# Optimization experiments

Hardware: AMD Instinct MI355X
Metric: run time of the kernel (lower is better)

## Reference

```python
import jax, jax.numpy as jnp
import numpy as np

N_NODES = 50000
N_FEAT = 256
HIDDEN = 256
N_EDGES = 800000


def gcn_conv(x, edge_index, W, b):
    """PyG GCNConv: out = D^-1/2 (A+I) D^-1/2 (x @ W) + b."""
    n = x.shape[0]
    loop = jnp.arange(n, dtype=edge_index.dtype)
    src = jnp.concatenate([edge_index[0], loop])  # [E+N]
    dst = jnp.concatenate([edge_index[1], loop])  # [E+N]
    deg = jax.ops.segment_sum(jnp.ones_like(dst, dtype=x.dtype), dst, num_segments=n)
    dinv = jnp.where(deg > 0, jax.lax.rsqrt(deg), 0.0)
    norm = dinv[src] * dinv[dst]                  # [E+N]
    h = x @ W                                     # [N, out]
    msg = h[src] * norm[:, None]                  # gather + scale
    out = jax.ops.segment_sum(msg, dst, num_segments=n)  # scatter-add
    return out + b


def setup_inputs() -> dict:
    key = jax.random.key(0)
    ks = jax.random.split(key, 8)
    x = jax.random.normal(ks[0], (N_NODES, N_FEAT), dtype=jnp.float32)
    train_pos_edge_index = jax.random.randint(ks[1], (2, N_EDGES), 0, N_NODES, dtype=jnp.int64)
    pos_edge_index = jax.random.randint(ks[2], (2, N_EDGES), 0, N_NODES, dtype=jnp.int64)
    neg_edge_index = jax.random.randint(ks[3], (2, N_EDGES), 0, N_NODES, dtype=jnp.int64)
    # Glorot-style init for GCN weights
    W1 = jax.random.normal(ks[4], (N_FEAT, HIDDEN), dtype=jnp.float32) * (1.0 / np.sqrt(N_FEAT))
    b1 = jnp.zeros((HIDDEN,), dtype=jnp.float32)
    W2 = jax.random.normal(ks[5], (HIDDEN, HIDDEN // 2), dtype=jnp.float32) * (1.0 / np.sqrt(HIDDEN))
    b2 = jnp.zeros((HIDDEN // 2,), dtype=jnp.float32)
    return {"x": x, "train_pos_edge_index": train_pos_edge_index,
            "pos_edge_index": pos_edge_index, "neg_edge_index": neg_edge_index,
            "W1": W1, "b1": b1, "W2": W2, "b2": b2}


def reference(x, train_pos_edge_index, pos_edge_index, neg_edge_index, W1, b1, W2, b2):
    # encode
    h = jax.nn.relu(gcn_conv(x, train_pos_edge_index, W1, b1))
    z = gcn_conv(h, train_pos_edge_index, W2, b2)  # [N, HIDDEN//2]
    # decode: dot product over concatenated pos+neg edges
    edge_index = jnp.concatenate([pos_edge_index, neg_edge_index], axis=-1)  # [2, 2E]
    logits = jnp.sum(z[edge_index[0]] * z[edge_index[1]], axis=-1)           # [2E]
    return logits
```

## Files before the change

### kernel.cpp

```cpp
#include <hip/hip_runtime.h>
#include <hip/hip_fp16.h>


#define NFEAT 256
#define HID   256
#define OUTF  128

typedef _Float16 f16x8 __attribute__((ext_vector_type(8)));
typedef _Float16 f16x2 __attribute__((ext_vector_type(2)));
typedef float    f32x4 __attribute__((ext_vector_type(4)));

__device__ __forceinline__ void wt_body(const float* __restrict__ W,
                                        __half* __restrict__ Wt,
                                        int K, int M, int bxx, int byy) {
    __shared__ float tile[32][33];
    int k0 = bxx * 32, m0 = byy * 32;
    int tx = threadIdx.x & 31, ty = threadIdx.x >> 5;
#pragma unroll
    for (int r = 0; r < 4; ++r)
        tile[ty + r * 8][tx] = W[(size_t)(k0 + ty + r * 8) * M + m0 + tx];
    __syncthreads();
#pragma unroll
    for (int r = 0; r < 4; ++r)
        Wt[(size_t)(m0 + ty + r * 8) * K + k0 + tx] = __float2half(tile[tx][ty + r * 8]);
}

__global__ __launch_bounds__(256) void k_prep(
        const float* __restrict__ W1, __half* __restrict__ W1t,
        const float* __restrict__ W2, __half* __restrict__ W2t,
        float* __restrict__ deg, int n) {
    int bid = blockIdx.x;
    if (bid < 64) { wt_body(W1, W1t, NFEAT, HID, bid & 7, bid >> 3); return; }
    bid -= 64;
    if (bid < 32) { wt_body(W2, W2t, HID, OUTF, bid & 7, bid >> 3); return; }
    bid -= 32;
    int i = bid * 256 + threadIdx.x;
    if (i < n) deg[i] = 1.0f;
}

__global__ void k_count_deg(const int* __restrict__ ei, float* __restrict__ deg, int E) {
    int e = blockIdx.x * blockDim.x + threadIdx.x;
    if (e < E) atomicAdd(&deg[ei[E + e]], 1.0f);
}

__global__ __launch_bounds__(1024) void k_scan1(
        const float* __restrict__ deg, int* __restrict__ excl,
        int* __restrict__ bsum, int n) {
    __shared__ int swsum[16];
    const int t = threadIdx.x, wave = t >> 6, lane = t & 63;
    const int i = blockIdx.x * 1024 + t;
    int v = (i < n) ? (int)deg[i] - 1 : 0;
    int sc = v;
#pragma unroll
    for (int off = 1; off < 64; off <<= 1) {
        int y = __shfl_up(sc, off);
        if (lane >= off) sc += y;
    }
    if (lane == 63) swsum[wave] = sc;
    __syncthreads();
    if (t < 16) {
        int w = swsum[t];
        int scw = w;
#pragma unroll
        for (int off = 1; off < 16; off <<= 1) {
            int y = __shfl_up(scw, off);
            if (t >= off) scw += y;
        }
        swsum[t] = scw - w;
        if (t == 15) bsum[blockIdx.x] = scw;
    }
    __syncthreads();
    if (i < n) excl[i] = swsum[wave] + (sc - v);
}

__global__ __launch_bounds__(256) void k_scan3(
        float* __restrict__ deg_dinv, const int* __restrict__ excl,
        const int* __restrict__ bsum, int* __restrict__ rowptr,
        int* __restrict__ cursor, int n, int nb) {
    __shared__ int pbs[65];
    const int t = threadIdx.x;
    if (t < 64) {
        int v = (t < nb) ? bsum[t] : 0;
        int sc = v;
#pragma unroll
        for (int off = 1; off < 64; off <<= 1) {
            int y = __shfl_up(sc, off);
            if (t >= off) sc += y;
        }
        pbs[t] = sc - v;
        if (t == 63) pbs[64] = sc;
    }
    __syncthreads();
    int i = blockIdx.x * 256 + t;
    if (i < n) {
        int rp = excl[i] + pbs[i >> 10];
        rowptr[i] = rp;
        cursor[i] = rp;
        deg_dinv[i] = rsqrtf(deg_dinv[i]);
    } else if (i == n) {
        rowptr[n] = pbs[64];
    }
}

__global__ void k_fill(const int* __restrict__ ei, int* __restrict__ cursor,
                       int* __restrict__ eidx, int E) {
    int e = blockIdx.x * blockDim.x + threadIdx.x;
    if (e < E) {
        int s = ei[e];
        int d = ei[E + e];
        int p = atomicAdd(&cursor[d], 1);
        eidx[p] = s;
    }
}

template <int MT, bool AF32, int SWL>
__global__ __launch_bounds__(256) void k_gemm_mfma(
        const void* __restrict__ Aptr, const __half* __restrict__ Wt,
        const float* __restrict__ dinv, __half* __restrict__ outp,
        int n, int K, int M) {
    constexpr int BM = 2 * MT * 16;
    __shared__ __half As[BM][40];
    __shared__ __half Bs[128][40];
    __shared__ __half Cs[4][16][72];

    const int t    = threadIdx.x;
    const int wave = t >> 6;
    const int lane = t & 63;
    const int row0 = blockIdx.x * BM;
    const int col0 = blockIdx.y * 128;
    const int wm = wave >> 1, wn = wave & 1;
    const int lr = lane & 15;
    const int kq = lane >> 4;

    f32x4 acc[MT][4];
#pragma unroll
    for (int i = 0; i < MT; ++i)
#pragma unroll
        for (int j = 0; j < 4; ++j) acc[i][j] = (f32x4){0.f, 0.f, 0.f, 0.f};

    for (int k0 = 0; k0 < K; k0 += 32) {
        if (AF32) {
            const float* A = (const float*)Aptr;
#pragma unroll
            for (int it = 0; it < BM * 8 / 256; ++it) {
                int q = t + it * 256;
                int r = q >> 3, c4 = q & 7;
                int gr = min(row0 + r, n - 1);
                float4 v = *(const float4*)&A[(size_t)gr * K + k0 + c4 * 4];
                __half2* dst = (__half2*)&As[r][c4 * 4];
                dst[0] = __floats2half2_rn(v.x, v.y);
                dst[1] = __floats2half2_rn(v.z, v.w);
            }
        } else {
            const __half* A = (const __half*)Aptr;
#pragma unroll
            for (int it = 0; it < BM * 4 / 256; ++it) {
                int q = t + it * 256;
                int r = q >> 2, c8 = q & 3;
                int gr = min(row0 + r, n - 1);
                *(float4*)&As[r][c8 * 8] = *(const float4*)&A[(size_t)gr * K + k0 + c8 * 8];
            }
        }
#pragma unroll
        for (int it = 0; it < 2; ++it) {
            int q = t + it * 256;
            int r = q >> 2, c8 = q & 3;
            *(float4*)&Bs[r][c8 * 8] = *(const float4*)&Wt[(size_t)(col0 + r) * K + k0 + c8 * 8];
        }
        __syncthreads();

        f16x8 b[4];
#pragma unroll
        for (int j = 0; j < 4; ++j)
            b[j] = *(const f16x8*)&Bs[wn * 64 + j * 16 + lr][kq * 8];
#pragma unroll
        for (int i = 0; i < MT; ++i) {
            f16x8 a = *(const f16x8*)&As[wm * MT * 16 + i * 16 + lr][kq * 8];
#pragma unroll
            for (int j = 0; j < 4; ++j)
                acc[i][j] = __builtin_amdgcn_mfma_f32_16x16x32_f16(a, b[j], acc[i][j], 0, 0, 0);
        }
        __syncthreads();
    }

    constexpr int SW = 1 << SWL;
#pragma unroll
    for (int i = 0; i < MT; ++i) {
        int gr0 = row0 + wm * MT * 16 + i * 16;
        float dv[4];
#pragma unroll
        for (int r = 0; r < 4; ++r)
            dv[r] = dinv[min(gr0 + kq * 4 + r, n - 1)];
        __syncthreads();
#pragma unroll
        for (int j = 0; j < 4; ++j)
#pragma unroll
            for (int r = 0; r < 4; ++r)
                Cs[wave][kq * 4 + r][j * 16 + lr] = __float2half(acc[i][j][r] * dv[r]);
        __syncthreads();
        int r1 = lane >> 3, c1 = (lane & 7) * 8;
#pragma unroll
        for (int h = 0; h < 2; ++h) {
            int grow = gr0 + r1 + h * 8;
            if (grow < n) {
                int col = col0 + wn * 64 + c1;
                size_t oidx = ((size_t)(col >> SWL) * n + grow) * SW + (col & (SW - 1));
                *(float4*)&outp[oidx] = *(const float4*)&Cs[wave][r1 + h * 8][c1];
            }
        }
    }
}

__global__ __launch_bounds__(256) void k_agg1(
        const int* __restrict__ rowptr, const int* __restrict__ eidx,
        const __half* __restrict__ g, const float* __restrict__ dinv,
        const float* __restrict__ bias, __half* __restrict__ out, int n) {
    const int node = (int)(((size_t)blockIdx.x * blockDim.x + threadIdx.x) >> 6);
    const int lane = threadIdx.x & 63;
    const int half = lane >> 5;
    const int fl   = lane & 31;
    if (node >= n) return;
    const int j0  = rowptr[node];
    const int end = rowptr[node + 1];
    const int last = end - 1;

    union U { float4 f; __half2 h[4]; };
    float acc[8] = {0.f, 0.f, 0.f, 0.f, 0.f, 0.f, 0.f, 0.f};
    {
        if (half == 0) {
            U u; u.f = *(const float4*)&g[(size_t)node * HID + fl * 8];
#pragma unroll
            for (int k = 0; k < 4; ++k) {
                float2 v = __half22float2(u.h[k]);
                acc[k * 2] += v.x; acc[k * 2 + 1] += v.y;
            }
        }
    }
    if (j0 < end) {
        int s0 = eidx[min(j0 + half, last)];
        int s1 = eidx[min(j0 + 2 + half, last)];
        for (int j = j0; j < end; j += 4) {
            int p0 = eidx[min(j + 4 + half, last)];
            int p1 = eidx[min(j + 6 + half, last)];
            U u0, u1;
            u0.f = *(const float4*)&g[(size_t)s0 * HID + fl * 8];
            u1.f = *(const float4*)&g[(size_t)s1 * HID + fl * 8];
            if (j + half < end) {
#pragma unroll
                for (int k = 0; k < 4; ++k) {
                    float2 v = __half22float2(u0.h[k]);
                    acc[k * 2] += v.x; acc[k * 2 + 1] += v.y;
                }
            }
            if (j + 2 + half < end) {
#pragma unroll
                for (int k = 0; k < 4; ++k) {
                    float2 v = __half22float2(u1.h[k]);
                    acc[k * 2] += v.x; acc[k * 2 + 1] += v.y;
                }
            }
            s0 = p0; s1 = p1;
        }
    }
#pragma unroll
    for (int k = 0; k < 8; ++k) acc[k] += __shfl_xor(acc[k], 32);
    if (half == 0) {
        const float sc = dinv[node];
        const int f0 = fl * 8;
        U r;
#pragma unroll
        for (int k = 0; k < 4; ++k) {
            float2 bb = *(const float2*)&bias[f0 + k * 2];
            r.h[k] = __floats2half2_rn(fmaxf(sc * acc[k * 2]     + bb.x, 0.f),
                                       fmaxf(sc * acc[k * 2 + 1] + bb.y, 0.f));
        }
        *(float4*)&out[(size_t)node * HID + f0] = r.f;
    }
}

__global__ __launch_bounds__(256) void k_agg2(
        const int* __restrict__ rowptr, const int* __restrict__ eidx,
        const __half* __restrict__ g, const float* __restrict__ dinv,
        const float* __restrict__ bias, __half* __restrict__ zs, int n) {
    const int node = (int)(((size_t)blockIdx.x * blockDim.x + threadIdx.x) >> 6);
    const int lane = threadIdx.x & 63;
    const int q    = lane >> 4;
    const int fl   = lane & 15;
    if (node >= n) return;
    const int j0  = rowptr[node];
    const int end = rowptr[node + 1];
    const int last = end - 1;

    union U { float4 f; __half2 h[4]; };
    float acc[8] = {0.f, 0.f, 0.f, 0.f, 0.f, 0.f, 0.f, 0.f};
    if (q == 0) {
        U u; u.f = *(const float4*)&g[(size_t)node * OUTF + fl * 8];
#pragma unroll
        for (int k = 0; k < 4; ++k) {
            float2 v = __half22float2(u.h[k]);
            acc[k * 2] += v.x; acc[k * 2 + 1] += v.y;
        }
    }
    if (j0 < end) {
        int s0 = eidx[min(j0 + q, last)];
        for (int j = j0; j < end; j += 4) {
            int p0 = eidx[min(j + 4 + q, last)];
            U u0; u0.f = *(const float4*)&g[(size_t)s0 * OUTF + fl * 8];
            if (j + q < end) {
#pragma unroll
                for (int k = 0; k < 4; ++k) {
                    float2 v = __half22float2(u0.h[k]);
                    acc[k * 2] += v.x; acc[k * 2 + 1] += v.y;
                }
            }
            s0 = p0;
        }
    }
#pragma unroll
    for (int k = 0; k < 8; ++k) {
        acc[k] += __shfl_xor(acc[k], 16);
        acc[k] += __shfl_xor(acc[k], 32);
    }
    if (q == 0) {
        const float sc = dinv[node];
        const int f0 = fl * 8;
        U r;
#pragma unroll
        for (int k = 0; k < 4; ++k) {
            float2 bb = *(const float2*)&bias[f0 + k * 2];
            r.h[k] = __floats2half2_rn(sc * acc[k * 2]     + bb.x,
                                       sc * acc[k * 2 + 1] + bb.y);
        }
        *(float4*)&zs[((size_t)(f0 >> 5) * n + node) * 32 + (f0 & 31)] = r.f;
    }
}

__global__ __launch_bounds__(256) void k_decode(
        const int* __restrict__ pos, const int* __restrict__ neg,
        const __half* __restrict__ zs, float* __restrict__ psum, int E, int n) {
    const int slice = blockIdx.x & 3;
    const int wv    = threadIdx.x >> 6;
    const int lane  = threadIdx.x & 63;
    const int eo    = lane >> 1;
    const int h     = lane & 1;
    int e = ((blockIdx.x >> 2) * 4 + wv) * 32 + eo;
    if (e >= 2 * E) return;
    int a, b;
    if (e < E) { a = pos[e];     b = pos[E + e]; }
    else       { a = neg[e - E]; b = neg[e];     }
    const __half* ra = zs + ((size_t)slice * n + a) * 32 + h * 16;
    const __half* rb = zs + ((size_t)slice * n + b) * 32 + h * 16;
    union U { float4 f; f16x2 d[4]; };
    U a0, a1, b0, b1;
    a0.f = *(const float4*)&ra[0];
    a1.f = *(const float4*)&ra[8];
    b0.f = *(const float4*)&rb[0];
    b1.f = *(const float4*)&rb[8];
    float p = 0.f;
#if __has_builtin(__builtin_amdgcn_fdot2)
#pragma unroll
    for (int k = 0; k < 4; ++k) p = __builtin_amdgcn_fdot2(a0.d[k], b0.d[k], p, false);
#pragma unroll
    for (int k = 0; k < 4; ++k) p = __builtin_amdgcn_fdot2(a1.d[k], b1.d[k], p, false);
#else
#pragma unroll
    for (int k = 0; k < 4; ++k) {
        p += (float)a0.d[k][0] * (float)b0.d[k][0] + (float)a0.d[k][1] * (float)b0.d[k][1];
        p += (float)a1.d[k][0] * (float)b1.d[k][0] + (float)a1.d[k][1] * (float)b1.d[k][1];
    }
#endif
    p += __shfl_xor(p, 1);
    if (h == 0)
        __builtin_nontemporal_store(p, &psum[(size_t)slice * 2 * E + e]);
}

__global__ void k_dsum(const float* __restrict__ psum, float* __restrict__ out, int n2e) {
    int e = blockIdx.x * blockDim.x + threadIdx.x;
    if (e < n2e) {
        float p0 = __builtin_nontemporal_load(&psum[e]);
        float p1 = __builtin_nontemporal_load(&psum[(size_t)n2e + e]);
        float p2 = __builtin_nontemporal_load(&psum[2 * (size_t)n2e + e]);
        float p3 = __builtin_nontemporal_load(&psum[3 * (size_t)n2e + e]);
        out[e] = (p0 + p1) + (p2 + p3);
    }
}

extern "C" void kernel_launch(void* const* d_in, const int* in_sizes, int n_in,
                              void* d_out, int out_size, void* d_ws, size_t ws_size,
                              hipStream_t stream) {
    const float* x   = (const float*)d_in[0];
    const int*   tei = (const int*)d_in[1];
    const int*   pos = (const int*)d_in[2];
    const int*   neg = (const int*)d_in[3];
    const float* W1  = (const float*)d_in[4];
    const float* b1  = (const float*)d_in[5];
    const float* W2  = (const float*)d_in[6];
    const float* b2  = (const float*)d_in[7];
    float* out = (float*)d_out;

    const int N = in_sizes[0] / NFEAT;
    const int E = in_sizes[1] / 2;
    const int NB = (N + 1023) / 1024;

    char* ws = (char*)d_ws;
    size_t off = 0;
    __half* g1h = (__half*)(ws + off);
    __half* g2h = (__half*)(ws + off);
    __half* zs  = (__half*)(ws + off + (size_t)N * OUTF * 2);
    off += (size_t)N * HID * 2;
    __half* h1h  = (__half*)(ws + off);
    float*  psum = (float*)(ws + off);
    off += (size_t)N * HID * 2;
    float*  dinv = (float*)(ws + off);  off += (size_t)N * 4;
    int* rowptr = (int*)(ws + off);     off += (size_t)(N + 1) * 4;
    int* cursor = (int*)(ws + off);     off += (size_t)N * 4;
    int* eidx   = (int*)(ws + off);     off += (size_t)E * 4;
    __half* W1t = (__half*)(ws + off);  off += (size_t)NFEAT * HID * 2;
    __half* W2t = (__half*)(ws + off);  off += (size_t)HID * OUTF * 2;
    int* excl   = (int*)(ws + off);     off += (size_t)N * 4;
    int* bsum   = (int*)(ws + off);     off += (size_t)(NB + 1) * 4;

    {
        int nbi = (N + 255) / 256;
        k_prep<<<64 + 32 + nbi, 256, 0, stream>>>(W1, W1t, W2, W2t, dinv, N);
    }

    k_count_deg<<<(E + 255) / 256, 256, 0, stream>>>(tei, dinv, E);
    k_scan1<<<NB, 1024, 0, stream>>>(dinv, excl, bsum, N);
    k_scan3<<<(N + 256) / 256, 256, 0, stream>>>(dinv, excl, bsum, rowptr, cursor, N, NB);
    k_fill<<<(E + 255) / 256, 256, 0, stream>>>(tei, cursor, eidx, E);

    {
        dim3 grid((N + 127) / 128, HID / 128);
        k_gemm_mfma<4, true, 8><<<grid, 256, 0, stream>>>(x, W1t, dinv, g1h, N, NFEAT, HID);
        int nblk = (int)(((size_t)N * 64 + 255) / 256);
        k_agg1<<<nblk, 256, 0, stream>>>(rowptr, eidx, g1h, dinv, b1, h1h, N);
    }

    {
        dim3 grid((N + 63) / 64, OUTF / 128);
        k_gemm_mfma<2, false, 7><<<grid, 256, 0, stream>>>(h1h, W2t, dinv, g2h, N, HID, OUTF);
        int nblk = (int)(((size_t)N * 64 + 255) / 256);
        k_agg2<<<nblk, 256, 0, stream>>>(rowptr, eidx, g2h, dinv, b2, zs, N);
    }

    {
        int nblk = 4 * ((2 * E + 127) / 128);
        k_decode<<<nblk, 256, 0, stream>>>(pos, neg, zs, psum, E, N);
        k_dsum<<<(2 * E + 255) / 256, 256, 0, stream>>>(psum, out, 2 * E);
    }
}
```

Baseline: 399.1 us.

## Store hidden features in 32-wide feature slices and aggregate per slice

```diff
diff --git a/kernel.cpp b/kernel.cpp
--- a/kernel.cpp
+++ b/kernel.cpp
@@ -113,7 +113,7 @@
     }
 }
 
-template <int MT, bool AF32, int SWL>
+template <int MT, bool AF32, bool ASL, int SWL>
 __global__ __launch_bounds__(256) void k_gemm_mfma(
         const void* __restrict__ Aptr, const __half* __restrict__ Wt,
         const float* __restrict__ dinv, __half* __restrict__ outp,
@@ -158,7 +158,14 @@
                 int q = t + it * 256;
                 int r = q >> 2, c8 = q & 3;
                 int gr = min(row0 + r, n - 1);
-                *(float4*)&As[r][c8 * 8] = *(const float4*)&A[(size_t)gr * K + k0 + c8 * 8];
+                size_t aidx;
+                if (ASL) {
+                    int kk = k0 + c8 * 8;
+                    aidx = ((size_t)(kk >> 5) * n + gr) * 32 + (kk & 31);
+                } else {
+                    aidx = (size_t)gr * K + k0 + c8 * 8;
+                }
+                *(float4*)&As[r][c8 * 8] = *(const float4*)&A[aidx];
             }
         }
 #pragma unroll
@@ -211,90 +218,26 @@
     }
 }
 
-__global__ __launch_bounds__(256) void k_agg1(
+template <int NS, bool RELU>
+__global__ __launch_bounds__(256) void k_aggs(
         const int* __restrict__ rowptr, const int* __restrict__ eidx,
         const __half* __restrict__ g, const float* __restrict__ dinv,
         const float* __restrict__ bias, __half* __restrict__ out, int n) {
-    const int node = (int)(((size_t)blockIdx.x * blockDim.x + threadIdx.x) >> 6);
-    const int lane = threadIdx.x & 63;
-    const int half = lane >> 5;
-    const int fl   = lane & 31;
+    const int slice = blockIdx.x & (NS - 1);
+    const int node  = (int)(((size_t)(blockIdx.x >> (NS == 8 ? 3 : 2)) * 4) + (threadIdx.x >> 6));
+    const int lane  = threadIdx.x & 63;
+    const int eo    = lane >> 2;
+    const int c     = lane & 3;
     if (node >= n) return;
+    const __half* gs = g + (size_t)slice * n * 32;
     const int j0  = rowptr[node];
     const int end = rowptr[node + 1];
     const int last = end - 1;
 
     union U { float4 f; __half2 h[4]; };
     float acc[8] = {0.f, 0.f, 0.f, 0.f, 0.f, 0.f, 0.f, 0.f};
-    {
-        if (half == 0) {
-            U u; u.f = *(const float4*)&g[(size_t)node * HID + fl * 8];
-#pragma unroll
-            for (int k = 0; k < 4; ++k) {
-                float2 v = __half22float2(u.h[k]);
-                acc[k * 2] += v.x; acc[k * 2 + 1] += v.y;
-            }
-        }
-    }
-    if (j0 < end) {
-        int s0 = eidx[min(j0 + half, last)];
-        int s1 = eidx[min(j0 + 2 + half, last)];
-        for (int j = j0; j < end; j += 4) {
-            int p0 = eidx[min(j + 4 + half, last)];
-            int p1 = eidx[min(j + 6 + half, last)];
-            U u0, u1;
-            u0.f = *(const float4*)&g[(size_t)s0 * HID + fl * 8];
-            u1.f = *(const float4*)&g[(size_t)s1 * HID + fl * 8];
-            if (j + half < end) {
-#pragma unroll
-                for (int k = 0; k < 4; ++k) {
-                    float2 v = __half22float2(u0.h[k]);
-                    acc[k * 2] += v.x; acc[k * 2 + 1] += v.y;
-                }
-            }
-            if (j + 2 + half < end) {
-#pragma unroll
-                for (int k = 0; k < 4; ++k) {
-                    float2 v = __half22float2(u1.h[k]);
-                    acc[k * 2] += v.x; acc[k * 2 + 1] += v.y;
-                }
-            }
-            s0 = p0; s1 = p1;
-        }
-    }
-#pragma unroll
-    for (int k = 0; k < 8; ++k) acc[k] += __shfl_xor(acc[k], 32);
-    if (half == 0) {
-        const float sc = dinv[node];
-        const int f0 = fl * 8;
-        U r;
-#pragma unroll
-        for (int k = 0; k < 4; ++k) {
-            float2 bb = *(const float2*)&bias[f0 + k * 2];
-            r.h[k] = __floats2half2_rn(fmaxf(sc * acc[k * 2]     + bb.x, 0.f),
-                                       fmaxf(sc * acc[k * 2 + 1] + bb.y, 0.f));
-        }
-        *(float4*)&out[(size_t)node * HID + f0] = r.f;
-    }
-}
-
-__global__ __launch_bounds__(256) void k_agg2(
-        const int* __restrict__ rowptr, const int* __restrict__ eidx,
-        const __half* __restrict__ g, const float* __restrict__ dinv,
-        const float* __restrict__ bias, __half* __restrict__ zs, int n) {
-    const int node = (int)(((size_t)blockIdx.x * blockDim.x + threadIdx.x) >> 6);
-    const int lane = threadIdx.x & 63;
-    const int q    = lane >> 4;
-    const int fl   = lane & 15;
-    if (node >= n) return;
-    const int j0  = rowptr[node];
-    const int end = rowptr[node + 1];
-    const int last = end - 1;
-
-    union U { float4 f; __half2 h[4]; };
-    float acc[8] = {0.f, 0.f, 0.f, 0.f, 0.f, 0.f, 0.f, 0.f};
-    if (q == 0) {
-        U u; u.f = *(const float4*)&g[(size_t)node * OUTF + fl * 8];
+    if (eo == 0) {
+        U u; u.f = *(const float4*)&gs[(size_t)node * 32 + c * 8];
 #pragma unroll
         for (int k = 0; k < 4; ++k) {
             float2 v = __half22float2(u.h[k]);
@@ -302,14 +245,14 @@
         }
     }
     if (j0 < end) {
-        int s0 = eidx[min(j0 + q, last)];
-        for (int j = j0; j < end; j += 4) {
-            int p0 = eidx[min(j + 4 + q, last)];
-            U u0; u0.f = *(const float4*)&g[(size_t)s0 * OUTF + fl * 8];
-            if (j + q < end) {
+        int s0 = eidx[min(j0 + eo, last)];
+        for (int j = j0; j < end; j += 16) {
+            int p0 = eidx[min(j + 16 + eo, last)];
+            U u; u.f = *(const float4*)&gs[(size_t)s0 * 32 + c * 8];
+            if (j + eo < end) {
 #pragma unroll
                 for (int k = 0; k < 4; ++k) {
-                    float2 v = __half22float2(u0.h[k]);
+                    float2 v = __half22float2(u.h[k]);
                     acc[k * 2] += v.x; acc[k * 2 + 1] += v.y;
                 }
             }
@@ -318,32 +261,37 @@
     }
 #pragma unroll
     for (int k = 0; k < 8; ++k) {
+        acc[k] += __shfl_xor(acc[k], 4);
+        acc[k] += __shfl_xor(acc[k], 8);
         acc[k] += __shfl_xor(acc[k], 16);
         acc[k] += __shfl_xor(acc[k], 32);
     }
-    if (q == 0) {
+    if (eo == 0) {
         const float sc = dinv[node];
-        const int f0 = fl * 8;
+        const int f0 = slice * 32 + c * 8;
         U r;
 #pragma unroll
         for (int k = 0; k < 4; ++k) {
             float2 bb = *(const float2*)&bias[f0 + k * 2];
-            r.h[k] = __floats2half2_rn(sc * acc[k * 2]     + bb.x,
-                                       sc * acc[k * 2 + 1] + bb.y);
-        }
-        *(float4*)&zs[((size_t)(f0 >> 5) * n + node) * 32 + (f0 & 31)] = r.f;
+            float x0 = sc * acc[k * 2]     + bb.x;
+            float x1 = sc * acc[k * 2 + 1] + bb.y;
+            if (RELU) { x0 = fmaxf(x0, 0.f); x1 = fmaxf(x1, 0.f); }
+            r.h[k] = __floats2half2_rn(x0, x1);
+        }
+        *(float4*)&out[((size_t)slice * n + node) * 32 + c * 8] = r.f;
     }
 }
 
 __global__ __launch_bounds__(256) void k_decode(
         const int* __restrict__ pos, const int* __restrict__ neg,
-        const __half* __restrict__ zs, float* __restrict__ psum, int E, int n) {
+        const __half* __restrict__ zs, float* __restrict__ psum,
+        int E, int n, int ebase) {
     const int slice = blockIdx.x & 3;
     const int wv    = threadIdx.x >> 6;
     const int lane  = threadIdx.x & 63;
     const int eo    = lane >> 1;
     const int h     = lane & 1;
-    int e = ((blockIdx.x >> 2) * 4 + wv) * 32 + eo;
+    int e = ebase + ((blockIdx.x >> 2) * 4 + wv) * 32 + eo;
     if (e >= 2 * E) return;
     int a, b;
     if (e < E) { a = pos[e];     b = pos[E + e]; }
@@ -404,11 +352,11 @@
 
     char* ws = (char*)d_ws;
     size_t off = 0;
-    __half* g1h = (__half*)(ws + off);
-    __half* g2h = (__half*)(ws + off);
+    __half* g1s = (__half*)(ws + off);
+    __half* g2s = (__half*)(ws + off);
     __half* zs  = (__half*)(ws + off + (size_t)N * OUTF * 2);
     off += (size_t)N * HID * 2;
-    __half* h1h  = (__half*)(ws + off);
+    __half* h1s  = (__half*)(ws + off);
     float*  psum = (float*)(ws + off);
     off += (size_t)N * HID * 2;
     float*  dinv = (float*)(ws + off);  off += (size_t)N * 4;
@@ -432,21 +380,22 @@
 
     {
         dim3 grid((N + 127) / 128, HID / 128);
-        k_gemm_mfma<4, true, 8><<<grid, 256, 0, stream>>>(x, W1t, dinv, g1h, N, NFEAT, HID);
-        int nblk = (int)(((size_t)N * 64 + 255) / 256);
-        k_agg1<<<nblk, 256, 0, stream>>>(rowptr, eidx, g1h, dinv, b1, h1h, N);
+        k_gemm_mfma<4, true, false, 5><<<grid, 256, 0, stream>>>(x, W1t, dinv, g1s, N, NFEAT, HID);
+        int nblk = 8 * ((N + 3) / 4);
+        k_aggs<8, true><<<nblk, 256, 0, stream>>>(rowptr, eidx, g1s, dinv, b1, h1s, N);
     }
 
     {
         dim3 grid((N + 63) / 64, OUTF / 128);
-        k_gemm_mfma<2, false, 7><<<grid, 256, 0, stream>>>(h1h, W2t, dinv, g2h, N, HID, OUTF);
-        int nblk = (int)(((size_t)N * 64 + 255) / 256);
-        k_agg2<<<nblk, 256, 0, stream>>>(rowptr, eidx, g2h, dinv, b2, zs, N);
+        k_gemm_mfma<2, false, true, 5><<<grid, 256, 0, stream>>>(h1s, W2t, dinv, g2s, N, HID, OUTF);
+        int nblk = 4 * ((N + 3) / 4);
+        k_aggs<4, false><<<nblk, 256, 0, stream>>>(rowptr, eidx, g2s, dinv, b2, zs, N);
     }
 
     {
-        int nblk = 4 * ((2 * E + 127) / 128);
-        k_decode<<<nblk, 256, 0, stream>>>(pos, neg, zs, psum, E, N);
+        int nblk = 4 * ((E + 127) / 128);
+        k_decode<<<nblk, 256, 0, stream>>>(pos, neg, zs, psum, E, N, 0);
+        k_decode<<<nblk, 256, 0, stream>>>(pos, neg, zs, psum, E, N, E);
         k_dsum<<<(2 * E + 255) / 256, 256, 0, stream>>>(psum, out, 2 * E);
     }
 }
```

New measurement: 506.8 us. 27.0% more time.
